# Kernel tuning notes

Measured on AMD Instinct MI355X. Metric: run time of the kernel, lower is better.

Reference implementation:

```python
import jax, jax.numpy as jnp
import numpy as np

B, T, D = 2, 2048, 1024
N_HEADS, D_HEAD, WINDOW = 16, 64, 256
SCALE = D_HEAD ** -0.5


def setup_inputs() -> dict:
    key = jax.random.key(0)
    k1, k2, k3 = jax.random.split(key, 3)
    x = jax.random.normal(k1, (B, T, D), dtype=jnp.float32)
    # torch Linear weights are [out_features, in_features], init std=0.02
    w_qkv = jax.random.normal(k2, (3 * N_HEADS * D_HEAD, D), dtype=jnp.float32) * 0.02
    w_out = jax.random.normal(k3, (D, N_HEADS * D_HEAD), dtype=jnp.float32) * 0.02
    return {"x": x, "w_qkv": w_qkv, "w_out": w_out}


def reference(x, w_qkv, w_out):
    b, t, d = x.shape
    qkv = jnp.einsum('btd,ed->bte', x, w_qkv)  # [B,T,3*H*Dh]
    q, k, v = jnp.split(qkv, 3, axis=-1)
    def heads(u):
        return u.reshape(b, t, N_HEADS, D_HEAD).transpose(0, 2, 1, 3)  # [B,H,T,Dh]
    q, k, v = heads(q), heads(k), heads(v)
    scores = jnp.einsum('bhqd,bhkd->bhqk', q, k) * SCALE  # [B,H,T,T]
    pos = jnp.arange(t)
    dist = pos[:, None] - pos[None, :]  # query - key
    allowed = (dist >= 0) & (dist < WINDOW)  # causal sliding window
    neg_inf = jnp.asarray(-jnp.inf, dtype=scores.dtype)
    scores = jnp.where(allowed[None, None], scores, neg_inf)
    attn = jax.nn.softmax(scores, axis=-1)
    out = jnp.einsum('bhqk,bhkd->bhqd', attn, v)  # [B,H,T,Dh]
    out = out.transpose(0, 2, 1, 3).reshape(b, t, N_HEADS * D_HEAD)
    return jnp.einsum('bte,de->btd', out, w_out)
```

## Files before the change

### kernel.cpp

```cpp
#include <hip/hip_runtime.h>
#include <hip/hip_bf16.h>

typedef unsigned short bfu;
typedef __attribute__((ext_vector_type(8))) short short8;
typedef __attribute__((ext_vector_type(4))) float floatx4;
typedef __attribute__((ext_vector_type(2))) __fp16 fp16x2;
typedef __attribute__((ext_vector_type(4))) _Float16 half4v;

#define B_ 2
#define T_ 2048
#define D_ 1024
#define NH 16
#define DH 64
#define WIN 256
#define QKV_COLS 3072
#define NX  (B_ * T_ * D_)
#define NWQ (QKV_COLS * D_)
#define NWO (D_ * D_)

__device__ __forceinline__ bfu f2b_bits(float f) {
  union { __hip_bfloat16 h; bfu u; } cv;
  cv.h = __float2bfloat16(f);
  return cv.u;
}

__device__ __forceinline__ void gl_lds16(const bfu* g, bfu* l) {
  __builtin_amdgcn_global_load_lds(
      (const __attribute__((address_space(1))) unsigned int*)g,
      (__attribute__((address_space(3))) unsigned int*)l, 16, 0, 0);
}

__global__ void cvt3_kernel(const float* __restrict__ x, const float* __restrict__ wq,
                            const float* __restrict__ wo, bfu* __restrict__ out) {
  int i = (blockIdx.x * 256 + threadIdx.x) * 4;
  const float* src;
  int off;
  if (i < NX)            { src = x;  off = 0; }
  else if (i < NX + NWQ) { src = wq; off = NX; }
  else                   { src = wo; off = NX + NWQ; }
  floatx4 v = *(const floatx4*)(src + (i - off));
  out[i + 0] = f2b_bits(v.x);
  out[i + 1] = f2b_bits(v.y);
  out[i + 2] = f2b_bits(v.z);
  out[i + 3] = f2b_bits(v.w);
}

template <int EPI, int TN>
__global__ __launch_bounds__(256) void gemm_bt_kernel(const bfu* __restrict__ A,
                                                      const bfu* __restrict__ Bm,
                                                      void* __restrict__ C,
                                                      int M, int N, int K) {
  constexpr int NJ = TN / 32;
  __shared__ __align__(16) bfu As[128][64];
  __shared__ __align__(16) bfu Bs[TN][64];
  const int tid = threadIdx.x;
  const int wave = tid >> 6, lane = tid & 63;
  const int quad = lane >> 4, cl = lane & 15;
  const int lr = lane >> 3, lg = lane & 7, sg = lg ^ lr;
  const int wm = (wave >> 1) * 64, wn = (wave & 1) * (TN / 2);
  const int m0 = blockIdx.y * 128, n0 = blockIdx.x * TN;

  floatx4 acc[4][NJ] = {};

  for (int k0 = 0; k0 < K; k0 += 64) {
    __syncthreads();
#pragma unroll
    for (int i = 0; i < 4; ++i) {
      const int row = i * 32 + wave * 8;
      gl_lds16(A + (size_t)(m0 + row + lr) * K + k0 + sg * 8, &As[row][0]);
    }
#pragma unroll
    for (int i = 0; i < TN / 32; ++i) {
      const int row = i * 32 + wave * 8;
      gl_lds16(Bm + (size_t)(n0 + row + lr) * K + k0 + sg * 8, &Bs[row][0]);
    }
    __syncthreads();
#pragma unroll
    for (int ks = 0; ks < 2; ++ks) {
      const int gsw = ks * 4 + quad;
      short8 af[4], bfr[NJ];
#pragma unroll
      for (int im = 0; im < 4; ++im)
        af[im] = *(const short8*)(&As[wm + im * 16 + cl][(gsw ^ (cl & 7)) << 3]);
#pragma unroll
      for (int in = 0; in < NJ; ++in)
        bfr[in] = *(const short8*)(&Bs[wn + in * 16 + cl][(gsw ^ (cl & 7)) << 3]);
#pragma unroll
      for (int im = 0; im < 4; ++im)
#pragma unroll
        for (int in = 0; in < NJ; ++in)
          acc[im][in] = __builtin_amdgcn_mfma_f32_16x16x32_bf16(af[im], bfr[in], acc[im][in], 0, 0, 0);
    }
  }
  const float qs = (EPI == 2 && n0 < 1024) ? 0.125f : 1.0f;
  const bool vf16 = (EPI == 2) && (n0 >= 2048);
#pragma unroll
  for (int im = 0; im < 4; ++im) {
#pragma unroll
    for (int r = 0; r < 4; ++r) {
      const size_t row = (size_t)(m0 + wm + im * 16 + quad * 4 + r);
#pragma unroll
      for (int in = 0; in < NJ; ++in) {
        const size_t idx = row * (size_t)N + (n0 + wn + in * 16 + cl);
        const float val = acc[im][in][r];
        if constexpr (EPI == 0) {
          ((float*)C)[idx] = val;
        } else {
          bfu bits;
          if (vf16) { union { _Float16 h; bfu u; } cv; cv.h = (_Float16)val; bits = cv.u; }
          else      { bits = f2b_bits(val * qs); }
          ((bfu*)C)[idx] = bits;
        }
      }
    }
  }
}

__global__ __launch_bounds__(512, 4) void swa_kernel(const bfu* __restrict__ qkv,
                                                     bfu* __restrict__ aout) {
  __shared__ __align__(16) bfu Qs[128][64];
  __shared__ __align__(16) bfu Ks[2][64][64];
  __shared__ __align__(16) bfu Vs[2][64][64];

  const int qt = blockIdx.x, h = blockIdx.y, b = blockIdx.z;
  const int tid = threadIdx.x, wave = tid >> 6, lane = tid & 63;
  const int quad = lane >> 4, cl = lane & 15;
  const int lr = lane >> 3, lg = lane & 7, sg = lg ^ lr;
  const int q0 = qt * 128;
  const bfu* qb = qkv + (size_t)b * T_ * QKV_COLS + h * DH;
  const bfu* kb = qb + 1024;
  const bfu* vb = qb + 2048;

  const int jt0 = (qt >= 2) ? 2 * qt - 4 : 0;
  const int njt = (2 * qt + 1) - jt0 + 1;

  const int vrow = tid >> 3;
  const int vcol = (tid & 7) * 8;

#pragma unroll
  for (int i = 0; i < 2; ++i) {
    const int row = wave * 16 + i * 8;
    gl_lds16(qb + (size_t)(q0 + row + lr) * QKV_COLS + sg * 8, &Qs[row][0]);
  }
  gl_lds16(kb + (size_t)(jt0 * 64 + wave * 8 + lr) * QKV_COLS + sg * 8, &Ks[0][wave * 8][0]);
  {
    union { short8 v; bfu u[8]; } t0;
    t0.v = *(const short8*)(vb + (size_t)(jt0 * 64 + vrow) * QKV_COLS + vcol);
#pragma unroll
    for (int e = 0; e < 8; ++e) {
      const int d = vcol + e;
      const int gp = ((vrow >> 2) + d + (d >> 3)) & 15;
      Vs[0][d][gp * 4 + (vrow & 3)] = t0.u[e];
    }
  }
  __syncthreads();

  float l_acc = 0.f;
  floatx4 acc[4] = {};
  const int ddc = cl + (cl >> 3);
  const int qw0 = q0 + wave * 16;

  for (int it = 0; it < njt; ++it) {
    const int cur = it & 1, nxt = cur ^ 1;
    const int k0 = (jt0 + it) * 64;
    const bool pf = (it + 1 < njt);

    union { short8 v; bfu u[8]; } vp;
    if (pf) {
      const int kn = k0 + 64;
      gl_lds16(kb + (size_t)(kn + wave * 8 + lr) * QKV_COLS + sg * 8, &Ks[nxt][wave * 8][0]);
      vp.v = *(const short8*)(vb + (size_t)(kn + vrow) * QKV_COLS + vcol);
    }

    bool live[4];
#pragma unroll
    for (int jk = 0; jk < 4; ++jk) {
      const int kg0 = k0 + jk * 16;
      live[jk] = (qw0 + 15 >= kg0) && (qw0 <= kg0 + 270);
    }

    floatx4 s[4] = {};
#pragma unroll
    for (int ks = 0; ks < 2; ++ks) {
      const int col = ((ks * 4 + quad) ^ (cl & 7)) << 3;
      short8 bq = *(const short8*)(&Qs[wave * 16 + cl][col]);
#pragma unroll
      for (int jk = 0; jk < 4; ++jk)
        if (live[jk]) {
          short8 ak = *(const short8*)(&Ks[cur][jk * 16 + cl][col]);
          s[jk] = __builtin_amdgcn_mfma_f32_16x16x32_bf16(ak, bq, s[jk], 0, 0, 0);
        }
    }

    const int qg = qw0 + cl;
    half4v af[4] = {};
#pragma unroll
    for (int jk = 0; jk < 4; ++jk) {
      if (!live[jk]) continue;
      float p[4];
#pragma unroll
      for (int r = 0; r < 4; ++r) {
        const int kg = k0 + jk * 16 + quad * 4 + r;
        const int dist = qg - kg;
        p[r] = (dist >= 0 && dist < WIN) ? __expf(s[jk][r]) : 0.f;
        l_acc += p[r];
      }
      union { fp16x2 h2[2]; half4v h4; } u;
      u.h2[0] = __builtin_amdgcn_cvt_pkrtz(p[0], p[1]);
      u.h2[1] = __builtin_amdgcn_cvt_pkrtz(p[2], p[3]);
      af[jk] = u.h4;
    }

#pragma unroll
    for (int kt = 0; kt < 4; ++kt) {
      if (!live[kt]) continue;
#pragma unroll
      for (int jd = 0; jd < 4; ++jd) {
        const int d = jd * 16 + cl;
        const int gp = (kt * 4 + quad + ddc + jd * 2) & 15;
        half4v bv = *(const half4v*)(&Vs[cur][d][gp * 4]);
        acc[jd] = __builtin_amdgcn_mfma_f32_16x16x16f16(af[kt], bv, acc[jd], 0, 0, 0);
      }
    }

    if (pf) {
#pragma unroll
      for (int e = 0; e < 8; ++e) {
        const int d = vcol + e;
        const int gp = ((vrow >> 2) + d + (d >> 3)) & 15;
        Vs[nxt][d][gp * 4 + (vrow & 3)] = vp.u[e];
      }
    }
    __syncthreads();
  }

  l_acc += __shfl_xor(l_acc, 16);
  l_acc += __shfl_xor(l_acc, 32);
  const float linv = 1.f / l_acc;
  float lq[4];
#pragma unroll
  for (int r = 0; r < 4; ++r) lq[r] = __shfl(linv, quad * 4 + r);

  bfu* ob = aout + (size_t)b * T_ * D_ + h * DH;
#pragma unroll
  for (int r = 0; r < 4; ++r) {
    const size_t row = (size_t)(q0 + wave * 16 + quad * 4 + r);
#pragma unroll
    for (int jd = 0; jd < 4; ++jd)
      ob[row * D_ + jd * 16 + cl] = f2b_bits(acc[jd][r] * lq[r]);
  }
}

extern "C" void kernel_launch(void* const* d_in, const int* in_sizes, int n_in,
                              void* d_out, int out_size, void* d_ws, size_t ws_size,
                              hipStream_t stream) {
  const float* x     = (const float*)d_in[0];
  const float* w_qkv = (const float*)d_in[1];
  const float* w_out = (const float*)d_in[2];
  float* out = (float*)d_out;
  char* ws = (char*)d_ws;

  bfu* xb    = (bfu*)(ws);
  bfu* wqkvb = (bfu*)(ws + (8ull << 20));
  bfu* woutb = (bfu*)(ws + (14ull << 20));
  bfu* qkvb  = (bfu*)(ws + (16ull << 20));
  bfu* attb  = (bfu*)(ws + (40ull << 20));

  cvt3_kernel<<<(NX + NWQ + NWO) / 1024, 256, 0, stream>>>(x, w_qkv, w_out, xb);

  gemm_bt_kernel<2, 128><<<dim3(QKV_COLS / 128, (B_ * T_) / 128), 256, 0, stream>>>(
      xb, wqkvb, qkvb, B_ * T_, QKV_COLS, D_);

  swa_kernel<<<dim3(T_ / 128, NH, B_), 512, 0, stream>>>(qkvb, attb);

  gemm_bt_kernel<0, 64><<<dim3(D_ / 64, (B_ * T_) / 128), 256, 0, stream>>>(
      attb, woutb, out, B_ * T_, D_, D_);
}
```

Measured before the change: 151.1 us.

## Replace QKV GEMM with 256x256-tile 8-wave ping-pong pipelined kernel

Adds a new QKV projection GEMM that uses 256x256 output tiles, 512 threads (8 waves) and double-buffered LDS. Global-to-LDS prefetch is split into four phases, each interleaved with an MFMA group, using explicit vmcnt waits, barriers and setprio. A grid swizzle groups blocks for L2 locality. The aim is to raise operand reuse and overlap memory with compute, but only 192 blocks launch (fewer than one wave of blocks across the CUs) and the large tiles raise register and LDS pressure.

```diff
diff --git a/kernel.cpp b/kernel.cpp
--- a/kernel.cpp
+++ b/kernel.cpp
@@ -29,6 +29,9 @@
       (const __attribute__((address_space(1))) unsigned int*)g,
       (__attribute__((address_space(3))) unsigned int*)l, 16, 0, 0);
 }
+
+#define FBARRIER() do { asm volatile("" ::: "memory"); \
+  __builtin_amdgcn_s_barrier(); asm volatile("" ::: "memory"); } while (0)
 
 __global__ void cvt3_kernel(const float* __restrict__ x, const float* __restrict__ wq,
                             const float* __restrict__ wo, bfu* __restrict__ out) {
@@ -116,6 +119,163 @@
   }
 }
 
+__global__ __launch_bounds__(512, 2) void gemm8p_qkv_kernel(const bfu* __restrict__ A,
+                                                            const bfu* __restrict__ Bm,
+                                                            bfu* __restrict__ C,
+                                                            int M, int N, int K) {
+  __shared__ __align__(16) bfu As[2][256][64];
+  __shared__ __align__(16) bfu Bs[2][256][64];
+  const int tid = threadIdx.x;
+  const int wave = tid >> 6, lane = tid & 63;
+  const int quad = lane >> 4, cl = lane & 15;
+  const int lr = lane >> 3, lg = lane & 7, sg = lg ^ lr;
+
+  const int cpx = gridDim.x >> 3;
+  const int swz = (blockIdx.x & 7) * cpx + (blockIdx.x >> 3);
+  const int ntile = N >> 8;
+  const int m0 = (swz / ntile) * 256, n0 = (swz % ntile) * 256;
+  const int wmRow = (wave >> 2) * 128;
+  const int wnCol = (wave & 3) * 64;
+
+  floatx4 acc[8][4] = {};
+  const int NT = K >> 6;
+
+  auto stageA = [&](int buf, int r0, int k0s) {
+    gl_lds16(A + (size_t)(m0 + r0 + lr) * K + k0s + sg * 8, &As[buf][r0][0]);
+  };
+  auto stageB = [&](int buf, int r0, int k0s) {
+    gl_lds16(Bm + (size_t)(n0 + r0 + lr) * K + k0s + sg * 8, &Bs[buf][r0][0]);
+  };
+  const int a0 = wave * 8;
+  const int b0 = (wave >> 2) * 64 + (wave & 3) * 8;
+
+  auto ldA = [&](int buf, int rbase, int ks) -> short8 {
+    return *(const short8*)(&As[buf][rbase + cl][((ks * 4 + quad) ^ (cl & 7)) << 3]);
+  };
+  auto ldB = [&](int buf, int rbase, int ks) -> short8 {
+    return *(const short8*)(&Bs[buf][rbase + cl][((ks * 4 + quad) ^ (cl & 7)) << 3]);
+  };
+
+  stageA(0, a0, 0);          stageA(0, 128 + a0, 0);
+  stageB(0, b0, 0);          stageB(0, 128 + b0, 0);
+  stageB(0, b0 + 32, 0);     stageB(0, 128 + b0 + 32, 0);
+  stageA(0, 64 + a0, 0);     stageA(0, 192 + a0, 0);
+  asm volatile("s_waitcnt vmcnt(4)" ::: "memory");
+  FBARRIER();
+
+  for (int t = 0; t < NT; ++t) {
+    const int cur = t & 1, nxt = cur ^ 1;
+    const int kn = (t + 1) << 6;
+    const bool pf = (t + 1 < NT);
+    short8 af[4][2], bf0[2][2], bf1[2][2];
+
+#pragma unroll
+    for (int ks = 0; ks < 2; ++ks) {
+#pragma unroll
+      for (int im = 0; im < 4; ++im) af[im][ks] = ldA(cur, wmRow + im * 16, ks);
+#pragma unroll
+      for (int in = 0; in < 2; ++in) bf0[in][ks] = ldB(cur, wnCol + in * 16, ks);
+    }
+    if (pf) {
+      stageA(nxt, a0, kn);      stageA(nxt, 128 + a0, kn);
+      stageB(nxt, b0, kn);      stageB(nxt, 128 + b0, kn);
+      asm volatile("s_waitcnt vmcnt(6)" ::: "memory");
+    } else {
+      asm volatile("s_waitcnt vmcnt(2)" ::: "memory");
+    }
+    FBARRIER();
+    __builtin_amdgcn_s_setprio(1);
+#pragma unroll
+    for (int ks = 0; ks < 2; ++ks)
+#pragma unroll
+      for (int im = 0; im < 4; ++im)
+#pragma unroll
+        for (int in = 0; in < 2; ++in)
+          acc[im][in] = __builtin_amdgcn_mfma_f32_16x16x32_bf16(af[im][ks], bf0[in][ks], acc[im][in], 0, 0, 0);
+    __builtin_amdgcn_s_setprio(0);
+    FBARRIER();
+
+#pragma unroll
+    for (int ks = 0; ks < 2; ++ks)
+#pragma unroll
+      for (int in = 0; in < 2; ++in) bf1[in][ks] = ldB(cur, wnCol + 32 + in * 16, ks);
+    if (pf) {
+      stageB(nxt, b0 + 32, kn); stageB(nxt, 128 + b0 + 32, kn);
+      asm volatile("s_waitcnt vmcnt(6)" ::: "memory");
+    } else {
+      asm volatile("s_waitcnt vmcnt(0)" ::: "memory");
+    }
+    FBARRIER();
+    __builtin_amdgcn_s_setprio(1);
+#pragma unroll
+    for (int ks = 0; ks < 2; ++ks)
+#pragma unroll
+      for (int im = 0; im < 4; ++im)
+#pragma unroll
+        for (int in = 0; in < 2; ++in)
+          acc[im][2 + in] = __builtin_amdgcn_mfma_f32_16x16x32_bf16(af[im][ks], bf1[in][ks], acc[im][2 + in], 0, 0, 0);
+    __builtin_amdgcn_s_setprio(0);
+    FBARRIER();
+
+#pragma unroll
+    for (int ks = 0; ks < 2; ++ks)
+#pragma unroll
+      for (int im = 0; im < 4; ++im) af[im][ks] = ldA(cur, wmRow + 64 + im * 16, ks);
+    if (pf) {
+      stageA(nxt, 64 + a0, kn); stageA(nxt, 192 + a0, kn);
+    }
+    FBARRIER();
+    __builtin_amdgcn_s_setprio(1);
+#pragma unroll
+    for (int ks = 0; ks < 2; ++ks)
+#pragma unroll
+      for (int im = 0; im < 4; ++im)
+#pragma unroll
+        for (int in = 0; in < 2; ++in)
+          acc[4 + im][2 + in] = __builtin_amdgcn_mfma_f32_16x16x32_bf16(af[im][ks], bf1[in][ks], acc[4 + im][2 + in], 0, 0, 0);
+    __builtin_amdgcn_s_setprio(0);
+    FBARRIER();
+
+    if (pf) asm volatile("s_waitcnt vmcnt(4)" ::: "memory");
+    FBARRIER();
+    __builtin_amdgcn_s_setprio(1);
+#pragma unroll
+    for (int ks = 0; ks < 2; ++ks)
+#pragma unroll
+      for (int im = 0; im < 4; ++im)
+#pragma unroll
+        for (int in = 0; in < 2; ++in)
+          acc[4 + im][in] = __builtin_amdgcn_mfma_f32_16x16x32_bf16(af[im][ks], bf0[in][ks], acc[4 + im][in], 0, 0, 0);
+    __builtin_amdgcn_s_setprio(0);
+    FBARRIER();
+  }
+
+  const float qs = (n0 < 1024) ? 0.125f : 1.0f;
+  const bool vf16 = (n0 >= 2048);
+#pragma unroll
+  for (int qm = 0; qm < 2; ++qm) {
+#pragma unroll
+    for (int im = 0; im < 4; ++im) {
+#pragma unroll
+      for (int r = 0; r < 4; ++r) {
+        const size_t row = (size_t)(m0 + wmRow + qm * 64 + im * 16 + quad * 4 + r);
+#pragma unroll
+        for (int qn = 0; qn < 2; ++qn) {
+#pragma unroll
+          for (int in = 0; in < 2; ++in) {
+            const size_t idx = row * (size_t)N + (n0 + wnCol + qn * 32 + in * 16 + cl);
+            const float val = acc[qm * 4 + im][qn * 2 + in][r];
+            bfu bits;
+            if (vf16) { union { _Float16 h; bfu u; } cv; cv.h = (_Float16)val; bits = cv.u; }
+            else      { bits = f2b_bits(val * qs); }
+            C[idx] = bits;
+          }
+        }
+      }
+    }
+  }
+}
+
 __global__ __launch_bounds__(512, 4) void swa_kernel(const bfu* __restrict__ qkv,
                                                      bfu* __restrict__ aout) {
   __shared__ __align__(16) bfu Qs[128][64];
@@ -268,8 +428,7 @@
 
   cvt3_kernel<<<(NX + NWQ + NWO) / 1024, 256, 0, stream>>>(x, w_qkv, w_out, xb);
 
-  gemm_bt_kernel<2, 128><<<dim3(QKV_COLS / 128, (B_ * T_) / 128), 256, 0, stream>>>(
-      xb, wqkvb, qkvb, B_ * T_, QKV_COLS, D_);
+  gemm8p_qkv_kernel<<<dim3(192), 512, 0, stream>>>(xb, wqkvb, qkvb, B_ * T_, QKV_COLS, D_);
 
   swa_kernel<<<dim3(T_ / 128, NH, B_), 512, 0, stream>>>(qkvb, attb);
 
```

New measurement: 153.9 us. Within noise of the previous version (+1.8%).
